# Kernel optimization log

Hardware: AMD Instinct MI355X
Metric: run time of the kernel (lower is better)

The kernel has to match this reference:

```python
import jax, jax.numpy as jnp
import numpy as np

B, S, N, F, H, E, L = 16, 64, 128, 16, 64, 1024, 2
NEG_SLOPE = 0.2


def _gat_layer(h, src, tgt, Wl, bl, Wr, br, att, bo):
    # h: [B,S,N,H]; src/tgt: [Et] (edges incl. self-loops)
    xl = jnp.einsum('bsnf,hf->bsnh', h, Wl) + bl
    xr = jnp.einsum('bsnf,hf->bsnh', h, Wr) + br
    e = xl[:, :, src] + xr[:, :, tgt]                       # [B,S,Et,H]
    e = jnp.where(e > 0, e, NEG_SLOPE * e)                  # leaky_relu(0.2)
    a = jnp.einsum('bseh,h->bse', e, att)                   # [B,S,Et]
    # segment softmax over target node (stable)
    m = jnp.full(a.shape[:2] + (N,), -jnp.inf, a.dtype).at[:, :, tgt].max(a)
    p = jnp.exp(a - m[:, :, tgt])
    z = jnp.zeros(a.shape[:2] + (N,), a.dtype).at[:, :, tgt].add(p)
    alpha = p / z[:, :, tgt]
    out = jnp.zeros_like(xl).at[:, :, tgt].add(alpha[..., None] * xl[:, :, src])
    return out + bo


def _forward(x, edge_index, in_W, in_b, gat_Wl, gat_bl, gat_Wr, gat_br,
             gat_att, gat_bias, gru_Wih, gru_Whh, gru_bih, gru_bhh,
             oh_W1, oh_b1, oh_W2, oh_b2, dh_W1, dh_b1, dh_W2, dh_b2):
    ar = jnp.arange(N, dtype=edge_index.dtype)
    ei = jnp.concatenate([edge_index, jnp.stack([ar, ar])], axis=1)  # add self-loops
    src, tgt = ei[0], ei[1]
    h = jnp.einsum('bsnf,hf->bsnh', x, in_W) + in_b          # input_proj
    for l in range(L):
        h = jax.nn.relu(_gat_layer(h, src, tgt, gat_Wl[l], gat_bl[l],
                                   gat_Wr[l], gat_br[l], gat_att[l], gat_bias[l]))
    # [B,S,N,H] -> sequences [B*N, S, H]; GRU, keep last state
    seqs = h.transpose(0, 2, 1, 3).reshape(B * N, S, H)

    def step(hprev, xt):
        gi = xt @ gru_Wih.T + gru_bih
        gh = hprev @ gru_Whh.T + gru_bhh
        ir, iz, inn = jnp.split(gi, 3, axis=-1)
        hr, hz, hn = jnp.split(gh, 3, axis=-1)
        r = jax.nn.sigmoid(ir + hr)
        zz = jax.nn.sigmoid(iz + hz)
        n = jnp.tanh(inn + r * hn)
        hnew = (1 - zz) * n + zz * hprev
        return hnew, None

    h0 = jnp.zeros((B * N, H), h.dtype)
    h_last, _ = jax.lax.scan(step, h0, seqs.transpose(1, 0, 2))
    h_last = h_last.reshape(B, N, H)

    def head(hh, W1, b1, W2, b2):
        return jax.nn.relu(hh @ W1.T + b1) @ W2.T + b2

    order = head(h_last, oh_W1, oh_b1, oh_W2, oh_b2)        # [B,N,1]
    demand = head(h_last, dh_W1, dh_b1, dh_W2, dh_b2)       # [B,N,1]
    return order, demand


def setup_inputs() -> dict:
    key = jax.random.key(0)
    ks = jax.random.split(key, 16)
    def g(i, shp, s=0.05):
        return (jax.random.normal(ks[i], shp) * s).astype(jnp.float32)
    x = jax.random.normal(ks[0], (B, S, N, F), dtype=jnp.float32)
    src = jax.random.randint(ks[1], (E,), 0, N)
    off = jax.random.randint(ks[2], (E,), 1, N)
    edge_index = jnp.stack([src, (src + off) % N]).astype(jnp.int32)  # no self-loops
    zf = lambda shp: jnp.zeros(shp, jnp.float32)
    return dict(
        x=x, edge_index=edge_index,
        in_W=g(3, (H, F)), in_b=zf((H,)),
        gat_Wl=g(4, (L, H, H)), gat_bl=zf((L, H)),
        gat_Wr=g(5, (L, H, H)), gat_br=zf((L, H)),
        gat_att=g(6, (L, H), 0.1), gat_bias=zf((L, H)),
        gru_Wih=g(7, (3 * H, H)), gru_Whh=g(8, (3 * H, H)),
        gru_bih=zf((3 * H,)), gru_bhh=zf((3 * H,)),
        oh_W1=g(9, (H // 2, H)), oh_b1=zf((H // 2,)),
        oh_W2=g(10, (1, H // 2)), oh_b2=zf((1,)),
        dh_W1=g(11, (H // 2, H)), dh_b1=zf((H // 2,)),
        dh_W2=g(12, (1, H // 2)), dh_b2=zf((1,)),
    )


def reference(x, edge_index, in_W, in_b, gat_Wl, gat_bl, gat_Wr, gat_br,
              gat_att, gat_bias, gru_Wih, gru_Whh, gru_bih, gru_bhh,
              oh_W1, oh_b1, oh_W2, oh_b2, dh_W1, dh_b1, dh_W2, dh_b2):
    return _forward(x, edge_index, in_W, in_b, gat_Wl, gat_bl, gat_Wr, gat_br,
                    gat_att, gat_bias, gru_Wih, gru_Whh, gru_bih, gru_bhh,
                    oh_W1, oh_b1, oh_W2, oh_b2, dh_W1, dh_b1, dh_W2, dh_b2)
```

## Files before the change

kernel.cpp:

```cpp
#include <hip/hip_runtime.h>
#include <math.h>

#define BB 16
#define SS 64
#define NN 128
#define FF 16
#define HH 64
#define EE 1024
#define ET 1152
#define LLAYERS 2
#define XPAD 65

__device__ __forceinline__ float readlane_f(float v, int k) {
  return __int_as_float(__builtin_amdgcn_readlane(__float_as_int(v), k));
}
__device__ __forceinline__ unsigned flipf(float f) {
  unsigned u = __float_as_uint(f);
  unsigned mask = (u & 0x80000000u) ? 0xFFFFFFFFu : 0x80000000u;
  return u ^ mask;
}
__device__ __forceinline__ float unflipf(unsigned u) {
  unsigned b = (u & 0x80000000u) ? (u ^ 0x80000000u) : ~u;
  return __uint_as_float(b);
}
__device__ __forceinline__ float sigmoidf_(float x) { return 1.f / (1.f + expf(-x)); }

__global__ void setup_csr_kernel(const int* __restrict__ ei,
                                 int* __restrict__ off,
                                 int* __restrict__ csrc,
                                 int* __restrict__ ctgt) {
  __shared__ int deg[NN], cur[NN], offs[NN + 1];
  int tid = threadIdx.x;
  if (tid < NN) deg[tid] = 0;
  __syncthreads();
  for (int e = tid; e < ET; e += 256) {
    int tg = (e < EE) ? ei[EE + e] : (e - EE);
    atomicAdd(&deg[tg], 1);
  }
  __syncthreads();
  if (tid == 0) {
    int s = 0;
    for (int i = 0; i < NN; ++i) { offs[i] = s; s += deg[i]; }
    offs[NN] = s;
  }
  __syncthreads();
  if (tid < NN) cur[tid] = offs[tid];
  if (tid <= NN) off[tid] = offs[tid];
  __syncthreads();
  for (int e = tid; e < ET; e += 256) {
    int sv, tg;
    if (e < EE) { sv = ei[e]; tg = ei[EE + e]; }
    else        { sv = e - EE; tg = e - EE; }
    int pos = atomicAdd(&cur[tg], 1);
    csrc[pos] = sv;
    ctgt[pos] = tg;
  }
}

__global__ __launch_bounds__(256) void input_proj_kernel(
    const float* __restrict__ x, const float* __restrict__ W,
    const float* __restrict__ bvec, float* __restrict__ h) {
  int lane = threadIdx.x & 63;
  int wid = threadIdx.x >> 6;
  float wreg[FF];
#pragma unroll
  for (int i = 0; i < FF / 4; ++i)
    *(float4*)&wreg[4 * i] = ((const float4*)(W + lane * FF))[i];
  float bias = bvec[lane];
  int row0 = __builtin_amdgcn_readfirstlane((blockIdx.x * 4 + wid) * 32);
#pragma unroll 2
  for (int r = 0; r < 32; ++r) {
    int row = row0 + r;
    const float* xr = x + row * FF;
    float acc = bias;
#pragma unroll
    for (int f = 0; f < FF; ++f) acc += xr[f] * wreg[f];
    h[row * HH + lane] = acc;
  }
}

__global__ __launch_bounds__(256) void xlxr_kernel(
    const float* __restrict__ hin,
    const float* __restrict__ Wl, const float* __restrict__ bl,
    const float* __restrict__ Wr, const float* __restrict__ br,
    float* __restrict__ xl, float* __restrict__ xr) {
  int lane = threadIdx.x & 63;
  int wid = (int)threadIdx.x >> 6;
  const float* W  = (wid & 1) ? Wr : Wl;
  const float* bv = (wid & 1) ? br : bl;
  float* outp     = (wid & 1) ? xr : xl;
  float w[HH];
#pragma unroll
  for (int i = 0; i < HH / 4; ++i)
    *(float4*)&w[4 * i] = ((const float4*)(W + lane * HH))[i];
  float bias = bv[lane];
  int row0 = __builtin_amdgcn_readfirstlane(blockIdx.x * 64 + (wid >> 1) * 32);
#pragma unroll 2
  for (int r = 0; r < 32; ++r) {
    const float* hrow = hin + (size_t)(row0 + r) * HH;
    float a0 = bias, a1 = 0.f, a2 = 0.f, a3 = 0.f;
#pragma unroll
    for (int f = 0; f < HH; f += 4) {
      a0 += hrow[f + 0] * w[f + 0];
      a1 += hrow[f + 1] * w[f + 1];
      a2 += hrow[f + 2] * w[f + 2];
      a3 += hrow[f + 3] * w[f + 3];
    }
    outp[(size_t)(row0 + r) * HH + lane] = (a0 + a1) + (a2 + a3);
  }
}

__global__ __launch_bounds__(256) void gat_edge_kernel(
    const float* __restrict__ xl_g, const float* __restrict__ xr_g,
    float* __restrict__ hout,
    const int* __restrict__ csr_off, const int* __restrict__ csr_src,
    const int* __restrict__ csr_tgt,
    const float* __restrict__ att, const float* __restrict__ bo) {
  __shared__ float xl_sh[NN * XPAD];
  __shared__ float xr_sh[NN * XPAD];
  __shared__ float p_sh[ET];
  __shared__ int st_sh[ET];
  __shared__ unsigned m_sh[NN];
  int tid = threadIdx.x, lane = tid & 63, wid = tid >> 6;
  int base = blockIdx.x * (NN * HH);

#pragma unroll 1
  for (int i = tid * 4; i < NN * HH; i += 256 * 4) {
    int row = i >> 6, h = i & 63;
    float4 vl = *(const float4*)(xl_g + base + i);
    float4 vr = *(const float4*)(xr_g + base + i);
    float* dl = xl_sh + row * XPAD + h;
    float* dr = xr_sh + row * XPAD + h;
    dl[0] = vl.x; dl[1] = vl.y; dl[2] = vl.z; dl[3] = vl.w;
    dr[0] = vr.x; dr[1] = vr.y; dr[2] = vr.z; dr[3] = vr.w;
  }
  for (int i = tid; i < ET; i += 256)
    st_sh[i] = csr_src[i] | (csr_tgt[i] << 16);
  if (tid < NN) m_sh[tid] = 0u;
  __syncthreads();

#pragma unroll 1
  for (int e = tid; e < ET; e += 256) {
    int st = st_sh[e];
    int s = st & 0xffff, tg = st >> 16;
    const float* xlr = xl_sh + s * XPAD;
    const float* xrr = xr_sh + tg * XPAD;
    float a0 = 0.f, a1 = 0.f, a2 = 0.f, a3 = 0.f;
#pragma unroll
    for (int h = 0; h < HH; h += 4) {
      float v0 = xlr[h + 0] + xrr[h + 0]; v0 = (v0 > 0.f) ? v0 : 0.2f * v0;
      float v1 = xlr[h + 1] + xrr[h + 1]; v1 = (v1 > 0.f) ? v1 : 0.2f * v1;
      float v2 = xlr[h + 2] + xrr[h + 2]; v2 = (v2 > 0.f) ? v2 : 0.2f * v2;
      float v3 = xlr[h + 3] + xrr[h + 3]; v3 = (v3 > 0.f) ? v3 : 0.2f * v3;
      a0 += v0 * att[h + 0];
      a1 += v1 * att[h + 1];
      a2 += v2 * att[h + 2];
      a3 += v3 * att[h + 3];
    }
    float a = (a0 + a1) + (a2 + a3);
    p_sh[e] = a;
    atomicMax(&m_sh[tg], flipf(a));
  }
  __syncthreads();

  for (int e = tid; e < ET; e += 256) {
    int tg = st_sh[e] >> 16;
    p_sh[e] = expf(p_sh[e] - unflipf(m_sh[tg]));
  }
  __syncthreads();

  float bo_l = bo[lane];
#pragma unroll 1
  for (int n = wid; n < NN; n += 4) {
    int o0 = __builtin_amdgcn_readfirstlane(csr_off[n]);
    int o1 = __builtin_amdgcn_readfirstlane(csr_off[n + 1]);
    float acc = 0.f, z = 0.f;
    for (int i = o0; i < o1; ++i) {
      float p = p_sh[i];
      int s = st_sh[i] & 0xffff;
      acc += p * xl_sh[s * XPAD + lane];
      z += p;
    }
    float o = acc / z + bo_l;
    hout[base + n * HH + lane] = fmaxf(o, 0.f);
  }
}

__device__ __forceinline__ void gemm_half(
    const float* __restrict__ hin, int base,
    const float* __restrict__ W, const float* __restrict__ bvec,
    float* __restrict__ out_sh, int half, int lane) {
  float wreg[HH];
#pragma unroll
  for (int i = 0; i < HH / 4; ++i)
    *(float4*)&wreg[4 * i] = ((const float4*)(W + lane * HH))[i];
  float bias = bvec[lane];
  int n0 = __builtin_amdgcn_readfirstlane(half * 64);
#pragma unroll 1
  for (int nd = 0; nd < 64; ++nd) {
    int node = n0 + nd;
    const float* hrow = hin + base + node * HH;
    float a0 = bias, a1 = 0.f, a2 = 0.f, a3 = 0.f;
#pragma unroll
    for (int f = 0; f < HH; f += 4) {
      a0 += hrow[f + 0] * wreg[f + 0];
      a1 += hrow[f + 1] * wreg[f + 1];
      a2 += hrow[f + 2] * wreg[f + 2];
      a3 += hrow[f + 3] * wreg[f + 3];
    }
    out_sh[node * HH + lane] = (a0 + a1) + (a2 + a3);
  }
}

__global__ __launch_bounds__(256) void gat_fused_kernel(
    const float* __restrict__ hin, float* __restrict__ hout,
    const int* __restrict__ csr_off, const int* __restrict__ csr_src,
    const int* __restrict__ csr_tgt,
    const float* __restrict__ Wl, const float* __restrict__ bl,
    const float* __restrict__ Wr, const float* __restrict__ br,
    const float* __restrict__ att, const float* __restrict__ bo) {
  __shared__ float xl_sh[NN * HH];
  __shared__ float xr_sh[NN * HH];
  __shared__ float p_sh[ET];
  __shared__ int st_sh[ET];
  __shared__ unsigned m_sh[NN];
  int tid = threadIdx.x, lane = tid & 63, wid = tid >> 6;
  int base = blockIdx.x * (NN * HH);

  for (int i = tid; i < ET; i += 256)
    st_sh[i] = csr_src[i] | (csr_tgt[i] << 16);
  if (tid < NN) m_sh[tid] = 0u;

  if (wid < 2) gemm_half(hin, base, Wl, bl, xl_sh, wid & 1, lane);
  else         gemm_half(hin, base, Wr, br, xr_sh, wid & 1, lane);

  float att_l = att[lane];
  float bo_l = bo[lane];
  __syncthreads();

#pragma unroll 1
  for (int e = wid; e < ET; e += 4) {
    int st = st_sh[e];
    int s = st & 0xffff, tg = st >> 16;
    float v = xl_sh[s * HH + lane] + xr_sh[tg * HH + lane];
    v = (v > 0.f) ? v : 0.2f * v;
    float prod = v * att_l;
#pragma unroll
    for (int mm = 32; mm; mm >>= 1) prod += __shfl_xor(prod, mm);
    if (lane == 0) {
      p_sh[e] = prod;
      atomicMax(&m_sh[tg], flipf(prod));
    }
  }
  __syncthreads();

  for (int e = tid; e < ET; e += 256) {
    int tg = st_sh[e] >> 16;
    p_sh[e] = expf(p_sh[e] - unflipf(m_sh[tg]));
  }
  __syncthreads();

#pragma unroll 1
  for (int n = wid; n < NN; n += 4) {
    int o0 = csr_off[n], o1 = csr_off[n + 1];
    float acc = 0.f, z = 0.f;
    for (int i = o0; i < o1; ++i) {
      float p = p_sh[i];
      int s = st_sh[i] & 0xffff;
      acc += p * xl_sh[s * HH + lane];
      z += p;
    }
    float o = acc / z + bo_l;
    hout[base + n * HH + lane] = fmaxf(o, 0.f);
  }
}

__global__ __launch_bounds__(128, 2) void gru_pc_kernel(
    const float* __restrict__ hbuf,
    const float* __restrict__ Wih, const float* __restrict__ Whh,
    const float* __restrict__ bih, const float* __restrict__ bhh,
    const float* __restrict__ oW1, const float* __restrict__ ob1,
    const float* __restrict__ oW2, const float* __restrict__ ob2,
    const float* __restrict__ dW1, const float* __restrict__ db1,
    const float* __restrict__ dW2, const float* __restrict__ db2,
    float* __restrict__ out) {
  int lane = threadIdx.x & 63;
  int w = (int)threadIdx.x >> 6;
  int seq = blockIdx.x;
  int b = seq >> 7, n = seq & (NN - 1);

  __shared__ float ring[2][3][HH];
  __shared__ float hsh[HH];

  const float* Wsel = w ? Whh : Wih;
  const float* Bsel = w ? bhh : bih;
  float wt[3][HH];
#pragma unroll
  for (int g = 0; g < 3; ++g) {
    const float4* src = (const float4*)(Wsel + (size_t)(g * 64 + lane) * HH);
#pragma unroll
    for (int i = 0; i < HH / 4; ++i)
      *(float4*)&wt[g][4 * i] = src[i];
  }
  float b_r = Bsel[lane], b_z = Bsel[64 + lane], b_n = Bsel[128 + lane];

  const float* xbase = hbuf + ((size_t)(b * SS) * NN + n) * HH;
  float hj = 0.f;

  if (w == 0) {
    float xv = xbase[lane];
    float ar0 = b_r, ar1 = 0.f, az0 = b_z, az1 = 0.f, an0 = b_n, an1 = 0.f;
#pragma unroll
    for (int k = 0; k < HH; k += 2) {
      float x0 = readlane_f(xv, k), x1 = readlane_f(xv, k + 1);
      ar0 += x0 * wt[0][k];     az0 += x0 * wt[1][k];     an0 += x0 * wt[2][k];
      ar1 += x1 * wt[0][k + 1]; az1 += x1 * wt[1][k + 1]; an1 += x1 * wt[2][k + 1];
    }
    ring[0][0][lane] = ar0 + ar1;
    ring[0][1][lane] = az0 + az1;
    ring[0][2][lane] = an0 + an1;
  }
  __syncthreads();

#pragma unroll 1
  for (int t = 0; t < SS; ++t) {
    if (w == 0) {
      if (t + 1 < SS) {
        const float* xr = xbase + (size_t)(t + 1) * NN * HH;
        float xv = xr[lane];
        float ar0 = b_r, ar1 = 0.f, az0 = b_z, az1 = 0.f, an0 = b_n, an1 = 0.f;
#pragma unroll
        for (int k = 0; k < HH; k += 2) {
          float x0 = readlane_f(xv, k), x1 = readlane_f(xv, k + 1);
          ar0 += x0 * wt[0][k];     az0 += x0 * wt[1][k];     an0 += x0 * wt[2][k];
          ar1 += x1 * wt[0][k + 1]; az1 += x1 * wt[1][k + 1]; an1 += x1 * wt[2][k + 1];
        }
        int slot = (t + 1) & 1;
        ring[slot][0][lane] = ar0 + ar1;
        ring[slot][1][lane] = az0 + az1;
        ring[slot][2][lane] = an0 + an1;
      }
    } else {
      int slot = t & 1;
      float gir = ring[slot][0][lane];
      float giz = ring[slot][1][lane];
      float gin = ring[slot][2][lane];
      float ar0 = b_r, ar1 = 0.f, az0 = b_z, az1 = 0.f, an0 = b_n, an1 = 0.f;
#pragma unroll
      for (int k = 0; k < HH; k += 2) {
        float h0 = readlane_f(hj, k), h1 = readlane_f(hj, k + 1);
        ar0 += h0 * wt[0][k];     az0 += h0 * wt[1][k];     an0 += h0 * wt[2][k];
        ar1 += h1 * wt[0][k + 1]; az1 += h1 * wt[1][k + 1]; an1 += h1 * wt[2][k + 1];
      }
      float ghr = ar0 + ar1, ghz = az0 + az1, ghn = an0 + an1;
      float rg = sigmoidf_(gir + ghr);
      float zg = sigmoidf_(giz + ghz);
      float ng = tanhf(gin + rg * ghn);
      hj = (1.f - zg) * ng + zg * hj;
    }
    __syncthreads();
  }

  if (w == 1) hsh[lane] = hj;
  __syncthreads();

  if (w == 1) {
    int half = lane >> 5, jp = lane & 31;
    const float* W1 = half ? dW1 : oW1;
    const float* b1 = half ? db1 : ob1;
    const float* W2 = half ? dW2 : oW2;
    const float* b2 = half ? db2 : ob2;
    float wv[HH];
#pragma unroll
    for (int i = 0; i < HH / 4; ++i)
      *(float4*)&wv[4 * i] = ((const float4*)(W1 + jp * HH))[i];
    float acc = b1[jp];
#pragma unroll
    for (int k = 0; k < HH; k += 4) {
      float4 hb = *(const float4*)(hsh + k);
      acc += hb.x * wv[k + 0];
      acc += hb.y * wv[k + 1];
      acc += hb.z * wv[k + 2];
      acc += hb.w * wv[k + 3];
    }
    float val = fmaxf(acc, 0.f) * W2[jp];
    val += __shfl_down(val, 16, 32);
    val += __shfl_down(val, 8, 32);
    val += __shfl_down(val, 4, 32);
    val += __shfl_down(val, 2, 32);
    val += __shfl_down(val, 1, 32);
    if (jp == 0) out[half * (BB * NN) + seq] = val + b2[0];
  }
}

extern "C" void kernel_launch(void* const* d_in, const int* in_sizes, int n_in,
                              void* d_out, int out_size, void* d_ws, size_t ws_size,
                              hipStream_t stream) {
  const float* x       = (const float*)d_in[0];
  const int*   ei      = (const int*)d_in[1];
  const float* in_W    = (const float*)d_in[2];
  const float* in_b    = (const float*)d_in[3];
  const float* gat_Wl  = (const float*)d_in[4];
  const float* gat_bl  = (const float*)d_in[5];
  const float* gat_Wr  = (const float*)d_in[6];
  const float* gat_br  = (const float*)d_in[7];
  const float* gat_att = (const float*)d_in[8];
  const float* gat_bias= (const float*)d_in[9];
  const float* gru_Wih = (const float*)d_in[10];
  const float* gru_Whh = (const float*)d_in[11];
  const float* gru_bih = (const float*)d_in[12];
  const float* gru_bhh = (const float*)d_in[13];
  const float* oh_W1   = (const float*)d_in[14];
  const float* oh_b1   = (const float*)d_in[15];
  const float* oh_W2   = (const float*)d_in[16];
  const float* oh_b2   = (const float*)d_in[17];
  const float* dh_W1   = (const float*)d_in[18];
  const float* dh_b1   = (const float*)d_in[19];
  const float* dh_W2   = (const float*)d_in[20];
  const float* dh_b2   = (const float*)d_in[21];
  float* out = (float*)d_out;

  char* ws = (char*)d_ws;
  size_t hfloats = (size_t)BB * SS * NN * HH;
  float* hbuf = (float*)ws;
  size_t off_csr = hfloats * sizeof(float);
  size_t off_buf = off_csr + (160 + 2 * ET) * sizeof(int);
  off_buf = (off_buf + 255) & ~(size_t)255;
  int* csr_off = (int*)(ws + off_csr);
  int* csr_src = csr_off + 160;
  int* csr_tgt = csr_src + ET;
  float* xlbuf = (float*)(ws + off_buf);
  float* xrbuf = xlbuf + hfloats;
  size_t need_gat = off_buf + 2 * hfloats * sizeof(float);
  bool big_gat = (ws_size >= need_gat);

  setup_csr_kernel<<<1, 256, 0, stream>>>(ei, csr_off, csr_src, csr_tgt);
  input_proj_kernel<<<(BB * SS * NN) / (4 * 32), 256, 0, stream>>>(x, in_W, in_b, hbuf);
  for (int l = 0; l < LLAYERS; ++l) {
    if (big_gat) {
      xlxr_kernel<<<(BB * SS * NN) / 64, 256, 0, stream>>>(
          hbuf, gat_Wl + l * HH * HH, gat_bl + l * HH,
          gat_Wr + l * HH * HH, gat_br + l * HH, xlbuf, xrbuf);
      gat_edge_kernel<<<BB * SS, 256, 0, stream>>>(
          xlbuf, xrbuf, hbuf, csr_off, csr_src, csr_tgt,
          gat_att + l * HH, gat_bias + l * HH);
    } else {
      gat_fused_kernel<<<BB * SS, 256, 0, stream>>>(
          hbuf, hbuf, csr_off, csr_src, csr_tgt,
          gat_Wl + l * HH * HH, gat_bl + l * HH,
          gat_Wr + l * HH * HH, gat_br + l * HH,
          gat_att + l * HH, gat_bias + l * HH);
    }
  }
  gru_pc_kernel<<<BB * NN, 128, 0, stream>>>(
      hbuf, gru_Wih, gru_Whh, gru_bih, gru_bhh,
      oh_W1, oh_b1, oh_W2, oh_b2, dh_W1, dh_b1, dh_W2, dh_b2, out);
}
```

Baseline: 692.5 us.

## Split GRU gates across three waves and precompute input projections into LDS

```diff
diff --git a/kernel.cpp b/kernel.cpp
--- a/kernel.cpp
+++ b/kernel.cpp
@@ -275,7 +275,7 @@
   }
 }
 
-__global__ __launch_bounds__(128, 2) void gru_pc_kernel(
+__global__ __launch_bounds__(192, 4) void gru_fused_kernel(
     const float* __restrict__ hbuf,
     const float* __restrict__ Wih, const float* __restrict__ Whh,
     const float* __restrict__ bih, const float* __restrict__ bhh,
@@ -284,87 +284,79 @@
     const float* __restrict__ dW1, const float* __restrict__ db1,
     const float* __restrict__ dW2, const float* __restrict__ db2,
     float* __restrict__ out) {
+  __shared__ float gi_sh[SS * 3 * HH];
+  __shared__ float exch[3 * HH];
+  __shared__ float hsh[HH];
+
   int lane = threadIdx.x & 63;
-  int w = (int)threadIdx.x >> 6;
+  int g = (int)threadIdx.x >> 6;
   int seq = blockIdx.x;
   int b = seq >> 7, n = seq & (NN - 1);
-
-  __shared__ float ring[2][3][HH];
-  __shared__ float hsh[HH];
-
-  const float* Wsel = w ? Whh : Wih;
-  const float* Bsel = w ? bhh : bih;
-  float wt[3][HH];
-#pragma unroll
-  for (int g = 0; g < 3; ++g) {
-    const float4* src = (const float4*)(Wsel + (size_t)(g * 64 + lane) * HH);
-#pragma unroll
-    for (int i = 0; i < HH / 4; ++i)
-      *(float4*)&wt[g][4 * i] = src[i];
-  }
-  float b_r = Bsel[lane], b_z = Bsel[64 + lane], b_n = Bsel[128 + lane];
-
-  const float* xbase = hbuf + ((size_t)(b * SS) * NN + n) * HH;
+  const float* xbase = hbuf + ((size_t)b * SS * NN + (size_t)n) * HH;
+
+  {
+    float w[HH];
+    const float4* wsrc = (const float4*)(Wih + (size_t)(g * 64 + lane) * HH);
+#pragma unroll
+    for (int i = 0; i < HH / 4; ++i) *(float4*)&w[4 * i] = wsrc[i];
+    float bias = bih[g * 64 + lane];
+    if (g == 0) hsh[lane] = 0.f;
+#pragma unroll 2
+    for (int t = 0; t < SS; ++t) {
+      const float* xr = xbase + (size_t)t * NN * HH;
+      float a0 = bias, a1 = 0.f, a2 = 0.f, a3 = 0.f;
+#pragma unroll
+      for (int k = 0; k < HH; k += 4) {
+        float4 xb = *(const float4*)(xr + k);
+        a0 += xb.x * w[k + 0];
+        a1 += xb.y * w[k + 1];
+        a2 += xb.z * w[k + 2];
+        a3 += xb.w * w[k + 3];
+      }
+      gi_sh[(t * 3 + g) * HH + lane] = (a0 + a1) + (a2 + a3);
+    }
+  }
+
+  float whh[HH];
+  {
+    const float4* wsrc = (const float4*)(Whh + (size_t)(g * 64 + lane) * HH);
+#pragma unroll
+    for (int i = 0; i < HH / 4; ++i) *(float4*)&whh[4 * i] = wsrc[i];
+  }
+  float bhg = bhh[g * 64 + lane];
   float hj = 0.f;
-
-  if (w == 0) {
-    float xv = xbase[lane];
-    float ar0 = b_r, ar1 = 0.f, az0 = b_z, az1 = 0.f, an0 = b_n, an1 = 0.f;
-#pragma unroll
-    for (int k = 0; k < HH; k += 2) {
-      float x0 = readlane_f(xv, k), x1 = readlane_f(xv, k + 1);
-      ar0 += x0 * wt[0][k];     az0 += x0 * wt[1][k];     an0 += x0 * wt[2][k];
-      ar1 += x1 * wt[0][k + 1]; az1 += x1 * wt[1][k + 1]; an1 += x1 * wt[2][k + 1];
-    }
-    ring[0][0][lane] = ar0 + ar1;
-    ring[0][1][lane] = az0 + az1;
-    ring[0][2][lane] = an0 + an1;
-  }
   __syncthreads();
 
 #pragma unroll 1
   for (int t = 0; t < SS; ++t) {
-    if (w == 0) {
-      if (t + 1 < SS) {
-        const float* xr = xbase + (size_t)(t + 1) * NN * HH;
-        float xv = xr[lane];
-        float ar0 = b_r, ar1 = 0.f, az0 = b_z, az1 = 0.f, an0 = b_n, an1 = 0.f;
-#pragma unroll
-        for (int k = 0; k < HH; k += 2) {
-          float x0 = readlane_f(xv, k), x1 = readlane_f(xv, k + 1);
-          ar0 += x0 * wt[0][k];     az0 += x0 * wt[1][k];     an0 += x0 * wt[2][k];
-          ar1 += x1 * wt[0][k + 1]; az1 += x1 * wt[1][k + 1]; an1 += x1 * wt[2][k + 1];
-        }
-        int slot = (t + 1) & 1;
-        ring[slot][0][lane] = ar0 + ar1;
-        ring[slot][1][lane] = az0 + az1;
-        ring[slot][2][lane] = an0 + an1;
-      }
-    } else {
-      int slot = t & 1;
-      float gir = ring[slot][0][lane];
-      float giz = ring[slot][1][lane];
-      float gin = ring[slot][2][lane];
-      float ar0 = b_r, ar1 = 0.f, az0 = b_z, az1 = 0.f, an0 = b_n, an1 = 0.f;
-#pragma unroll
-      for (int k = 0; k < HH; k += 2) {
-        float h0 = readlane_f(hj, k), h1 = readlane_f(hj, k + 1);
-        ar0 += h0 * wt[0][k];     az0 += h0 * wt[1][k];     an0 += h0 * wt[2][k];
-        ar1 += h1 * wt[0][k + 1]; az1 += h1 * wt[1][k + 1]; an1 += h1 * wt[2][k + 1];
-      }
-      float ghr = ar0 + ar1, ghz = az0 + az1, ghn = an0 + an1;
-      float rg = sigmoidf_(gir + ghr);
-      float zg = sigmoidf_(giz + ghz);
-      float ng = tanhf(gin + rg * ghn);
-      hj = (1.f - zg) * ng + zg * hj;
-    }
+    float gi_g = gi_sh[(t * 3 + g) * HH + lane];
+    float a0 = bhg, a1 = 0.f, a2 = 0.f, a3 = 0.f;
+#pragma unroll
+    for (int k = 0; k < HH; k += 4) {
+      float4 hb = *(const float4*)(hsh + k);
+      a0 += hb.x * whh[k + 0];
+      a1 += hb.y * whh[k + 1];
+      a2 += hb.z * whh[k + 2];
+      a3 += hb.w * whh[k + 3];
+    }
+    float gh = (a0 + a1) + (a2 + a3);
+    exch[g * HH + lane] = (g < 2) ? (gi_g + gh) : gh;
     __syncthreads();
-  }
-
-  if (w == 1) hsh[lane] = hj;
-  __syncthreads();
-
-  if (w == 1) {
+    if (g == 0) {
+      float sr  = exch[lane];
+      float sz  = exch[HH + lane];
+      float hn  = exch[2 * HH + lane];
+      float gin = gi_sh[(t * 3 + 2) * HH + lane];
+      float r = sigmoidf_(sr);
+      float z = sigmoidf_(sz);
+      float nn_ = tanhf(gin + r * hn);
+      hj = (1.f - z) * nn_ + z * hj;
+      hsh[lane] = hj;
+    }
+    __syncthreads();
+  }
+
+  if (g == 0) {
     int half = lane >> 5, jp = lane & 31;
     const float* W1 = half ? dW1 : oW1;
     const float* b1 = half ? db1 : ob1;
@@ -452,7 +444,7 @@
           gat_att + l * HH, gat_bias + l * HH);
     }
   }
-  gru_pc_kernel<<<BB * NN, 128, 0, stream>>>(
+  gru_fused_kernel<<<BB * NN, 192, 0, stream>>>(
       hbuf, gru_Wih, gru_Whh, gru_bih, gru_bhh,
       oh_W1, oh_b1, oh_W2, oh_b2, dh_W1, dh_b1, dh_W2, dh_b2, out);
 }
```

After: 807.2 us. 16.6% more time.
